# Kernel tuning notes

Measured on AMD Instinct MI355X. Metric: run time of the kernel, lower is better.

## Reference

```python
import jax, jax.numpy as jnp
import numpy as np

B, S, D, H = 4, 2048, 768, 8
HD = D // H
EPS = 1e-5
NEG = -1e9


def setup_inputs() -> dict:
    key = jax.random.key(0)
    ks = jax.random.split(key, 12)
    s = 1.0 / np.sqrt(D)
    inp = {
        "hidden_states": jax.random.normal(ks[0], (B, S, D), dtype=jnp.float32),
        "anchor_mask": jax.random.bernoulli(ks[1], 0.5, (B, S)),
        "ln_g": jnp.ones((D,), jnp.float32),
        "ln_b": jnp.zeros((D,), jnp.float32),
        "Wq": jax.random.uniform(ks[2], (D, D), jnp.float32, -s, s),
        "bq": jax.random.uniform(ks[3], (D,), jnp.float32, -s, s),
        "Wk": jax.random.uniform(ks[4], (D, D), jnp.float32, -s, s),
        "bk": jax.random.uniform(ks[5], (D,), jnp.float32, -s, s),
        "Wv": jax.random.uniform(ks[6], (D, D), jnp.float32, -s, s),
        "bv": jax.random.uniform(ks[7], (D,), jnp.float32, -s, s),
        "Wo": jax.random.uniform(ks[8], (D, D), jnp.float32, -s, s),
        "bo": jax.random.uniform(ks[9], (D,), jnp.float32, -s, s),
    }
    return inp


def reference(hidden_states, anchor_mask, ln_g, ln_b, Wq, bq, Wk, bk, Wv, bv, Wo, bo):
    # LayerNorm (per-token, so applying to all tokens == applying to gathered anchors)
    mu = jnp.mean(hidden_states, axis=-1, keepdims=True)
    var = jnp.mean(jnp.square(hidden_states - mu), axis=-1, keepdims=True)
    x = (hidden_states - mu) * jax.lax.rsqrt(var + EPS) * ln_g + ln_b

    # QKV projections: torch Linear is x @ W.T + b
    q = (jnp.einsum('bsd,ed->bse', x, Wq) + bq).reshape(B, S, H, HD)
    k = (jnp.einsum('bsd,ed->bse', x, Wk) + bk).reshape(B, S, H, HD)
    v = (jnp.einsum('bsd,ed->bse', x, Wv) + bv).reshape(B, S, H, HD)

    scale = 1.0 / np.sqrt(HD)
    scores = jnp.einsum('bqhd,bkhd->bhqk', q, k) * scale
    # keys restricted to anchor positions (equivalent to the gather)
    key_mask = anchor_mask[:, None, None, :]  # (B,1,1,S)
    scores = jnp.where(key_mask, scores, NEG)
    attn = jax.nn.softmax(scores, axis=-1)  # dropout is identity in eval

    out = jnp.einsum('bhqk,bkhd->bqhd', attn, v).reshape(B, S, D)
    out = jnp.einsum('bsd,ed->bse', out, Wo) + bo
    # scatter back: zeros at non-anchor positions
    return out * anchor_mask[:, :, None].astype(out.dtype)
```

## Files before the change

### kernel.cpp

```cpp
#include <hip/hip_runtime.h>
#include <math.h>

#define S_LEN 2048
#define D_DIM 768
#define NH 8
#define HD 96
#define NTOK 8192

typedef short bf16x8 __attribute__((ext_vector_type(8)));
typedef float f32x4 __attribute__((ext_vector_type(4)));
typedef float f32x16 __attribute__((ext_vector_type(16)));
typedef unsigned int u32x2 __attribute__((ext_vector_type(2)));
typedef unsigned int u32x4 __attribute__((ext_vector_type(4)));

__device__ __forceinline__ f32x4 mfma16(bf16x8 a, bf16x8 b, f32x4 c) {
    return __builtin_amdgcn_mfma_f32_16x16x32_bf16(a, b, c, 0, 0, 0);
}
__device__ __forceinline__ f32x16 mfma32(bf16x8 a, bf16x8 b, f32x16 c) {
    return __builtin_amdgcn_mfma_f32_32x32x16_bf16(a, b, c, 0, 0, 0);
}

__device__ __forceinline__ unsigned short f2bf(float f) {
    unsigned int u = __float_as_uint(f);
    u += 0x7fffu + ((u >> 16) & 1u);
    return (unsigned short)(u >> 16);
}

__device__ __forceinline__ unsigned int cvtpk(float lo, float hi) {
    unsigned int r;
    asm("v_cvt_pk_bf16_f32 %0, %1, %2" : "=v"(r) : "v"(lo), "v"(hi));
    return r;
}

__device__ __forceinline__ void gl_lds16(const unsigned short* g, unsigned short* l) {
    __builtin_amdgcn_global_load_lds(
        (const __attribute__((address_space(1))) unsigned int*)g,
        (__attribute__((address_space(3))) unsigned int*)l, 16, 0, 0);
}

#define TILE_SHORTS 6144
#define BH_SHORTS   196608

__global__ __launch_bounds__(256) void prep_kernel(
    const unsigned char* __restrict__ mb, int* __restrict__ idx, int* __restrict__ cnt,
    const float* __restrict__ Wq, const float* __restrict__ Wk,
    const float* __restrict__ Wv, const float* __restrict__ Wo,
    unsigned short* __restrict__ W4b, float* __restrict__ out)
{
    const int bi = blockIdx.x;
    const int t  = threadIdx.x;

    if (bi < 4) {
        __shared__ int red[4];
        __shared__ int warp_tot[4];
        const int b = bi;
        int s = 0;
        for (int i = t; i < NTOK; i += 256) s += (int)mb[i];
        for (int off = 32; off > 0; off >>= 1) s += __shfl_down(s, off, 64);
        if ((t & 63) == 0) red[t >> 6] = s;
        __syncthreads();
        const int total = red[0] + red[1] + red[2] + red[3];
        const int mode = (total > 20000) ? 2 : ((total > 2500) ? 1 : 0);
        const int*   mi = (const int*)mb;
        const float* mf = (const float*)mb;
        const int p0 = t * 8;
        int av = 0, c = 0;
        #pragma unroll
        for (int j = 0; j < 8; ++j) {
            const int g = b * S_LEN + p0 + j;
            bool a;
            if (mode == 2)      a = (mf[g] != 0.0f);
            else if (mode == 1) a = (mb[g] != 0);
            else                a = (mi[g] != 0);
            if (a) { av |= (1 << j); ++c; }
        }
        const int lane = t & 63, w = t >> 6;
        int v = c;
        #pragma unroll
        for (int off = 1; off < 64; off <<= 1) {
            const int u = __shfl_up(v, off, 64);
            if (lane >= off) v += u;
        }
        if (lane == 63) warp_tot[w] = v;
        __syncthreads();
        int wbase = 0;
        for (int i = 0; i < w; ++i) wbase += warp_tot[i];
        int o = wbase + v - c;
        #pragma unroll
        for (int j = 0; j < 8; ++j)
            if (av & (1 << j)) idx[b * S_LEN + (o++)] = p0 + j;
        if (t == 255) cnt[b] = wbase + v;
    } else {
        const int i = bi - 4;
        const int w = i / 288, blk = i % 288;
        const float* src = (w == 0) ? Wq : (w == 1) ? Wk : (w == 2) ? Wv : Wo;
        const int base = (blk * 256 + t) * 8;
        const float4 a = *(const float4*)&src[base];
        const float4 c = *(const float4*)&src[base + 4];
        uint4 u;
        u.x = (unsigned int)f2bf(a.x) | ((unsigned int)f2bf(a.y) << 16);
        u.y = (unsigned int)f2bf(a.z) | ((unsigned int)f2bf(a.w) << 16);
        u.z = (unsigned int)f2bf(c.x) | ((unsigned int)f2bf(c.y) << 16);
        u.w = (unsigned int)f2bf(c.z) | ((unsigned int)f2bf(c.w) << 16);
        *(uint4*)&W4b[(size_t)w * 589824 + base] = u;
    }
}

__global__ __launch_bounds__(256) void ln_gather_kernel(
    const float* __restrict__ H, const float* __restrict__ g,
    const float* __restrict__ bta, const int* __restrict__ idx,
    const int* __restrict__ cnt, unsigned short* __restrict__ X)
{
    const int b = blockIdx.y;
    const int w = threadIdx.x >> 6, lane = threadIdx.x & 63;
    const int r = blockIdx.x * 4 + w;
    if (r >= cnt[b]) return;
    const int slot = b * S_LEN + r;
    const int p = idx[slot];
    const float* hr = H + (size_t)(b * S_LEN + p) * D_DIM;
    unsigned short* xr = X + (size_t)slot * D_DIM;

    float4 v[3];
    #pragma unroll
    for (int q = 0; q < 3; ++q)
        v[q] = *(const float4*)&hr[lane * 4 + q * 256];

    float s = 0.0f, ss = 0.0f;
    #pragma unroll
    for (int q = 0; q < 3; ++q) {
        s  += v[q].x + v[q].y + v[q].z + v[q].w;
        ss += v[q].x * v[q].x + v[q].y * v[q].y
            + v[q].z * v[q].z + v[q].w * v[q].w;
    }
    #pragma unroll
    for (int off = 32; off > 0; off >>= 1) {
        s  += __shfl_xor(s,  off, 64);
        ss += __shfl_xor(ss, off, 64);
    }
    const float mu   = s * (1.0f / D_DIM);
    const float var  = ss * (1.0f / D_DIM) - mu * mu;
    const float rstd = rsqrtf(var + 1e-5f);

    #pragma unroll
    for (int q = 0; q < 3; ++q) {
        const int d0 = lane * 4 + q * 256;
        const float4 gv = *(const float4*)&g[d0];
        const float4 bv = *(const float4*)&bta[d0];
        uint2 u;
        u.x = (unsigned int)f2bf((v[q].x - mu) * rstd * gv.x + bv.x)
            | ((unsigned int)f2bf((v[q].y - mu) * rstd * gv.y + bv.y) << 16);
        u.y = (unsigned int)f2bf((v[q].z - mu) * rstd * gv.z + bv.z)
            | ((unsigned int)f2bf((v[q].w - mu) * rstd * gv.w + bv.w) << 16);
        *(uint2*)&xr[d0] = u;
    }
}

__global__ __launch_bounds__(256) void gemm_bf16(
    const unsigned short* __restrict__ A,
    const unsigned short* __restrict__ W4,
    const float* __restrict__ b0, const float* __restrict__ b1,
    const float* __restrict__ b2,
    const int* __restrict__ cnt, const int* __restrict__ idx,
    unsigned short* __restrict__ Qo, unsigned short* __restrict__ Kp,
    unsigned short* __restrict__ Vp, float* __restrict__ Fo,
    int oproj)
{
    const int bx = blockIdx.x;
    const int z  = oproj ? 0 : (bx % 3);
    const int nx = oproj ? bx : (bx / 3);
    const int m0 = blockIdx.y * 64;
    const int b  = m0 >> 11;
    const int rbase = m0 & (S_LEN - 1);
    const int nc = cnt[b];
    if (rbase >= nc) return;
    const int n0 = nx * 128;
    const unsigned short* W = W4 + (size_t)z * 589824;
    const float* bias = (z == 0) ? b0 : (z == 1 ? b1 : b2);

    __shared__ unsigned short Al[2][64 * 32];
    __shared__ unsigned short Bl[2][128 * 32];

    const int t = threadIdx.x;
    const int srow = t >> 2, sg = t & 3;
    const int ra0 = b * S_LEN + min(rbase + srow, nc - 1);
    const unsigned short* gA0 = A + (size_t)ra0 * 768 + sg * 8;
    const unsigned short* gB0 = W + (size_t)(n0 + srow)      * 768 + sg * 8;
    const unsigned short* gB1 = W + (size_t)(n0 + srow + 64) * 768 + sg * 8;
    const int t8 = t * 8;

    const int w = t >> 6, lane = t & 63;
    const int l15 = lane & 15, quad = lane >> 4;
    const int mh = (w & 1) * 32, nh2 = (w >> 1) * 64;

    f32x4 acc[2][4] = {};

    int aoff[2], boff[4];
    #pragma unroll
    for (int i = 0; i < 2; ++i) aoff[i] = (mh  + i * 16 + l15) * 32 + quad * 8;
    #pragma unroll
    for (int i = 0; i < 4; ++i) boff[i] = (nh2 + i * 16 + l15) * 32 + quad * 8;

    gl_lds16(gA0, &Al[0][t8]);
    gl_lds16(gB0, &Bl[0][t8]);
    gl_lds16(gB1, &Bl[0][2048 + t8]);
    asm volatile("s_waitcnt vmcnt(0)" ::: "memory");
    __builtin_amdgcn_s_barrier();
    __builtin_amdgcn_sched_barrier(0);

    for (int it = 0; it < 24; ++it) {
        const int cur = it & 1;
        if (it + 1 < 24) {
            const int k1 = (it + 1) * 32;
            gl_lds16(gA0 + k1, &Al[cur ^ 1][t8]);
            gl_lds16(gB0 + k1, &Bl[cur ^ 1][t8]);
            gl_lds16(gB1 + k1, &Bl[cur ^ 1][2048 + t8]);
            asm volatile("s_waitcnt vmcnt(3)" ::: "memory");
        } else {
            asm volatile("s_waitcnt vmcnt(0)" ::: "memory");
        }
        __builtin_amdgcn_s_barrier();
        __builtin_amdgcn_sched_barrier(0);

        bf16x8 af[2], bfr[4];
        #pragma unroll
        for (int i = 0; i < 2; ++i) af[i]  = *(const bf16x8*)(&Al[cur][aoff[i]]);
        #pragma unroll
        for (int i = 0; i < 4; ++i) bfr[i] = *(const bf16x8*)(&Bl[cur][boff[i]]);
        #pragma unroll
        for (int ms = 0; ms < 2; ++ms)
            #pragma unroll
            for (int ns = 0; ns < 4; ++ns)
                acc[ms][ns] = mfma16(af[ms], bfr[ns], acc[ms][ns]);

        __builtin_amdgcn_sched_barrier(0);
        __builtin_amdgcn_s_barrier();
    }

    if (!oproj) {
        if (z == 0) {
            #pragma unroll
            for (int ns = 0; ns < 4; ++ns) {
                const int n = n0 + nh2 + ns * 16 + l15;
                const float bv = bias[n];
                #pragma unroll
                for (int ms = 0; ms < 2; ++ms) {
                    const int ml = mh + ms * 16 + quad * 4;
                    #pragma unroll
                    for (int r = 0; r < 4; ++r) {
                        const int slot = b * S_LEN + rbase + ml + r;
                        Qo[(size_t)slot * 768 + n] = f2bf(acc[ms][ns][r] + bv);
                    }
                }
            }
        } else if (z == 1) {
            #pragma unroll
            for (int ns = 0; ns < 4; ++ns) {
                const int n = n0 + nh2 + ns * 16 + l15;
                const int h = n / 96, d = n - h * 96;
                const float bv = bias[n];
                unsigned short* base = Kp + (size_t)(b * 8 + h) * BH_SHORTS;
                const int dseg = d >> 3, dlo = d & 7;
                #pragma unroll
                for (int ms = 0; ms < 2; ++ms) {
                    const int ml = mh + ms * 16 + quad * 4;
                    #pragma unroll
                    for (int r = 0; r < 4; ++r) {
                        const int tok = rbase + ml + r;
                        const int kt = tok >> 6, tk = tok & 63;
                        const int g16 = tk >> 4, lr = tk & 15;
                        base[(size_t)kt * TILE_SHORTS +
                             (g16 * 192 + dseg * 16 + lr) * 8 + dlo] =
                            (tok < nc) ? f2bf(acc[ms][ns][r] + bv)
                                       : (unsigned short)0;
                    }
                }
            }
        } else {
            #pragma unroll
            for (int ns = 0; ns < 4; ++ns) {
                const int n = n0 + nh2 + ns * 16 + l15;
                const int h = n / 96, d = n - h * 96;
                const float bv = bias[n];
                unsigned short* base = Vp + (size_t)(b * 8 + h) * BH_SHORTS;
                const int dg = d >> 4, l16 = d & 15;
                #pragma unroll
                for (int ms = 0; ms < 2; ++ms) {
                    const int ml = mh + ms * 16 + quad * 4;
                    const int k = rbase + ml;
                    const int kt = k >> 6, tk = k & 63;
                    const int kseg = tk >> 3, klo = tk & 7;
                    const unsigned short h0 =
                        (k + 0 < nc) ? f2bf(acc[ms][ns][0] + bv) : (unsigned short)0;
                    const unsigned short h1 =
                        (k + 1 < nc) ? f2bf(acc[ms][ns][1] + bv) : (unsigned short)0;
                    const unsigned short h2 =
                        (k + 2 < nc) ? f2bf(acc[ms][ns][2] + bv) : (unsigned short)0;
                    const unsigned short h3 =
                        (k + 3 < nc) ? f2bf(acc[ms][ns][3] + bv) : (unsigned short)0;
                    uint2 u;
                    u.x = (unsigned int)h0 | ((unsigned int)h1 << 16);
                    u.y = (unsigned int)h2 | ((unsigned int)h3 << 16);
                    *(uint2*)&base[(size_t)kt * TILE_SHORTS +
                                   (dg * 128 + kseg * 16 + l16) * 8 + klo] = u;
                }
            }
        }
    } else {
        #pragma unroll
        for (int ns = 0; ns < 4; ++ns) {
            const int n = n0 + nh2 + ns * 16 + l15;
            const float bv = bias[n];
            #pragma unroll
            for (int ms = 0; ms < 2; ++ms) {
                const int ml = mh + ms * 16 + quad * 4;
                #pragma unroll
                for (int r = 0; r < 4; ++r) {
                    const int rloc = rbase + ml + r;
                    if (rloc < nc) {
                        const int orow = b * S_LEN + idx[b * S_LEN + rloc];
                        Fo[(size_t)orow * 768 + n] = acc[ms][ns][r] + bv;
                    }
                }
            }
        }
    }
}

__global__ __launch_bounds__(256) void attn_mfma(
    const unsigned short* __restrict__ Q,
    const unsigned short* __restrict__ Kp,
    const unsigned short* __restrict__ Vp,
    const int* __restrict__ cnt,
    unsigned short* __restrict__ O)
{
    const int bh = blockIdx.x & 31;
    const int b  = bh >> 3, h = bh & 7;
    const int q0 = (blockIdx.x >> 5) * 32;
    const int nk = cnt[b];
    if (q0 >= nk) return;

    __shared__ f32x4 CMB4[2][64][13];

    const int t = threadIdx.x, w = t >> 6, lane = t & 63;
    const int l15 = lane & 15;
    const int gh  = (lane >> 4) & 1;
    const int hi  = lane >> 5;
    const int q32 = lane & 31;
    const int bS  = b * S_LEN;
    const float CE = 0.14724459f;

    const unsigned short* Kg = Kp + (size_t)(b * 8 + h) * BH_SHORTS;
    const unsigned short* Vg = Vp + (size_t)(b * 8 + h) * BH_SHORTS;

    const unsigned short* qrow = Q + (size_t)(bS + q0 + q32) * 768 + h * 96 + hi * 8;
    bf16x8 qf[6];
    #pragma unroll
    for (int ks = 0; ks < 6; ++ks) qf[ks] = *(const bf16x8*)(qrow + ks * 16);

    const int kb0 = (gh * 192 + hi * 16 + l15) * 8;
    const int vb0 = (gh * 128 + hi * 16 + l15) * 8;

    float ls0 = 0.0f, ls1 = 0.0f;
    f32x16 oacc[3] = {};

    const int kts = (nk + 63) >> 6;

    for (int kt = w; kt < kts; kt += 4) {
        const unsigned short* Kt = Kg + (size_t)kt * TILE_SHORTS + kb0;
        const unsigned short* Vt = Vg + (size_t)kt * TILE_SHORTS + vb0;

        #pragma unroll
        for (int s = 0; s < 2; ++s) {
            bf16x8 kf[6];
            #pragma unroll
            for (int ks = 0; ks < 6; ++ks)
                kf[ks] = *(const bf16x8*)(Kt + (s * 384 + ks * 32) * 8);
            f32x16 sa = {};
            __builtin_amdgcn_s_setprio(1);
            #pragma unroll
            for (int ks = 0; ks < 6; ++ks) sa = mfma32(kf[ks], qf[ks], sa);
            __builtin_amdgcn_s_setprio(0);

            unsigned int wv[8];
            #pragma unroll
            for (int j = 0; j < 8; ++j) {
                const float e0 = exp2f(sa[2 * j]     * CE);
                const float e1 = exp2f(sa[2 * j + 1] * CE);
                if (j & 1) ls1 += e0 + e1; else ls0 += e0 + e1;
                wv[j] = cvtpk(e0, e1);
            }
            const u32x2 r02 = __builtin_amdgcn_permlane32_swap(wv[0], wv[2], false, false);
            const u32x2 r13 = __builtin_amdgcn_permlane32_swap(wv[1], wv[3], false, false);
            const u32x2 r46 = __builtin_amdgcn_permlane32_swap(wv[4], wv[6], false, false);
            const u32x2 r57 = __builtin_amdgcn_permlane32_swap(wv[5], wv[7], false, false);
            const u32x4 pw0 = { r02.x, r13.x, r02.y, r13.y };
            const u32x4 pw1 = { r46.x, r57.x, r46.y, r57.y };
            const bf16x8 pb0 = __builtin_bit_cast(bf16x8, pw0);
            const bf16x8 pb1 = __builtin_bit_cast(bf16x8, pw1);

            const int kkb = s * 2;
            __builtin_amdgcn_s_setprio(1);
            #pragma unroll
            for (int dg = 0; dg < 3; ++dg) {
                const bf16x8 v0 = *(const bf16x8*)(Vt + (dg * 256 + kkb * 32) * 8);
                const bf16x8 v1 = *(const bf16x8*)(Vt + (dg * 256 + (kkb + 1) * 32) * 8);
                oacc[dg] = mfma32(v0, pb0, oacc[dg]);
                oacc[dg] = mfma32(v1, pb1, oacc[dg]);
            }
            __builtin_amdgcn_s_setprio(0);
        }
    }

    float lsum = ls0 + ls1;
    lsum += __shfl_xor(lsum, 32);

    if (w >= 2) {
        f32x4* dst = CMB4[w - 2][lane];
        #pragma unroll
        for (int dg = 0; dg < 3; ++dg)
            #pragma unroll
            for (int m = 0; m < 4; ++m) {
                const f32x4 p = { oacc[dg][4 * m],     oacc[dg][4 * m + 1],
                                  oacc[dg][4 * m + 2], oacc[dg][4 * m + 3] };
                dst[dg * 4 + m] = p;
            }
        const f32x4 tl = { lsum, 0.0f, 0.0f, 0.0f };
        dst[12] = tl;
    }
    __syncthreads();
    if (w < 2) {
        const f32x4* src = CMB4[w][lane];
        #pragma unroll
        for (int dg = 0; dg < 3; ++dg)
            #pragma unroll
            for (int m = 0; m < 4; ++m) {
                const f32x4 p = src[dg * 4 + m];
                #pragma unroll
                for (int j = 0; j < 4; ++j) oacc[dg][4 * m + j] += p[j];
            }
        lsum += src[12][0];
    }
    __syncthreads();
    if (w == 1) {
        f32x4* dst = CMB4[0][lane];
        #pragma unroll
        for (int dg = 0; dg < 3; ++dg)
            #pragma unroll
            for (int m = 0; m < 4; ++m) {
                const f32x4 p = { oacc[dg][4 * m],     oacc[dg][4 * m + 1],
                                  oacc[dg][4 * m + 2], oacc[dg][4 * m + 3] };
                dst[dg * 4 + m] = p;
            }
        const f32x4 tl = { lsum, 0.0f, 0.0f, 0.0f };
        dst[12] = tl;
    }
    __syncthreads();
    if (w > 0) return;

    {
        const f32x4* src = CMB4[0][lane];
        #pragma unroll
        for (int dg = 0; dg < 3; ++dg)
            #pragma unroll
            for (int m = 0; m < 4; ++m) {
                const f32x4 p = src[dg * 4 + m];
                #pragma unroll
                for (int j = 0; j < 4; ++j) oacc[dg][4 * m + j] += p[j];
            }
        lsum += src[12][0];
    }
    lsum -= (float)((kts << 6) - nk);

    const int qi = q0 + q32;
    if (qi < nk) {
        const float rl = 1.0f / lsum;
        unsigned short* og = O + (size_t)(bS + qi) * 768 + h * 96;
        #pragma unroll
        for (int dg = 0; dg < 3; ++dg) {
            #pragma unroll
            for (int m = 0; m < 4; ++m) {
                uint2 u;
                u.x = cvtpk(oacc[dg][4 * m]     * rl, oacc[dg][4 * m + 1] * rl);
                u.y = cvtpk(oacc[dg][4 * m + 2] * rl, oacc[dg][4 * m + 3] * rl);
                *(uint2*)&og[dg * 32 + m * 8 + hi * 4] = u;
            }
        }
    }
}

extern "C" void kernel_launch(void* const* d_in, const int* in_sizes, int n_in,
                              void* d_out, int out_size, void* d_ws, size_t ws_size,
                              hipStream_t stream)
{
    const float* hs  = (const float*)d_in[0];
    const unsigned char* am = (const unsigned char*)d_in[1];
    const float* lng = (const float*)d_in[2];
    const float* lnb = (const float*)d_in[3];
    const float* Wq  = (const float*)d_in[4];
    const float* bq  = (const float*)d_in[5];
    const float* Wk  = (const float*)d_in[6];
    const float* bk  = (const float*)d_in[7];
    const float* Wv  = (const float*)d_in[8];
    const float* bv  = (const float*)d_in[9];
    const float* Wo  = (const float*)d_in[10];
    const float* bo  = (const float*)d_in[11];

    char* ws = (char*)d_ws;
    const size_t BUF = (size_t)NTOK * 768 * 2;
    int* idx = (int*)ws;
    int* cnt = (int*)(ws + 32768);
    unsigned short* xb  = (unsigned short*)(ws + 65536);
    unsigned short* Qb  = (unsigned short*)(ws + 65536 + BUF);
    unsigned short* Kpb = (unsigned short*)(ws + 65536 + 2 * BUF);
    unsigned short* Vpb = (unsigned short*)(ws + 65536 + 3 * BUF);
    unsigned short* W4b = (unsigned short*)(ws + 65536 + 4 * BUF);
    unsigned short* Ob  = xb;
    float* out = (float*)d_out;

    prep_kernel<<<dim3(1156), dim3(256), 0, stream>>>(
        am, idx, cnt, Wq, Wk, Wv, Wo, W4b, out);

    ln_gather_kernel<<<dim3(512, 4), dim3(256), 0, stream>>>(hs, lng, lnb, idx, cnt, xb);

    gemm_bf16<<<dim3(18, 128, 1), dim3(256), 0, stream>>>(
        xb, W4b, bq, bk, bv, cnt, idx, Qb, Kpb, Vpb, nullptr, 0);

    attn_mfma<<<dim3(2048), dim3(256), 0, stream>>>(Qb, Kpb, Vpb, cnt, Ob);

    gemm_bf16<<<dim3(6, 128, 1), dim3(256), 0, stream>>>(
        Ob, W4b + (size_t)3 * 589824, bo, bo, bo, cnt, idx,
        nullptr, nullptr, nullptr, out, 1);
}
```

Measured before the change: 191.2 us.

## Process two 32-query tiles per attention block to reuse K/V fragments

Each attention block now handles 64 query rows, as two 32-row sub-tiles, instead of 32. Every K and V fragment loaded from global memory feeds MFMAs for both sub-tiles, which halves K/V traffic per query. The grid is halved to match. The cost is doubled accumulator and score registers, which may lower occupancy, fewer blocks to balance across CUs, and a larger shared-memory reduction buffer.

```diff
diff --git a/kernel.cpp b/kernel.cpp
--- a/kernel.cpp
+++ b/kernel.cpp
@@ -335,11 +335,11 @@
 {
     const int bh = blockIdx.x & 31;
     const int b  = bh >> 3, h = bh & 7;
-    const int q0 = (blockIdx.x >> 5) * 32;
+    const int q0 = (blockIdx.x >> 5) * 64;
     const int nk = cnt[b];
     if (q0 >= nk) return;
 
-    __shared__ f32x4 CMB4[2][64][13];
+    __shared__ f32x4 CMB4[2][2][64][13];
 
     const int t = threadIdx.x, w = t >> 6, lane = t & 63;
     const int l15 = lane & 15;
@@ -352,16 +352,20 @@
     const unsigned short* Kg = Kp + (size_t)(b * 8 + h) * BH_SHORTS;
     const unsigned short* Vg = Vp + (size_t)(b * 8 + h) * BH_SHORTS;
 
-    const unsigned short* qrow = Q + (size_t)(bS + q0 + q32) * 768 + h * 96 + hi * 8;
-    bf16x8 qf[6];
-    #pragma unroll
-    for (int ks = 0; ks < 6; ++ks) qf[ks] = *(const bf16x8*)(qrow + ks * 16);
+    bf16x8 qf[2][6];
+    #pragma unroll
+    for (int qs = 0; qs < 2; ++qs) {
+        const unsigned short* qrow =
+            Q + (size_t)(bS + q0 + qs * 32 + q32) * 768 + h * 96 + hi * 8;
+        #pragma unroll
+        for (int ks = 0; ks < 6; ++ks) qf[qs][ks] = *(const bf16x8*)(qrow + ks * 16);
+    }
 
     const int kb0 = (gh * 192 + hi * 16 + l15) * 8;
     const int vb0 = (gh * 128 + hi * 16 + l15) * 8;
 
-    float ls0 = 0.0f, ls1 = 0.0f;
-    f32x16 oacc[3] = {};
+    float ls[2][2] = {};
+    f32x16 oacc0[3] = {}, oacc1[3] = {};
 
     const int kts = (nk + 63) >> 6;
 
@@ -375,28 +379,36 @@
             #pragma unroll
             for (int ks = 0; ks < 6; ++ks)
                 kf[ks] = *(const bf16x8*)(Kt + (s * 384 + ks * 32) * 8);
-            f32x16 sa = {};
+            f32x16 sa0 = {}, sa1 = {};
             __builtin_amdgcn_s_setprio(1);
             #pragma unroll
-            for (int ks = 0; ks < 6; ++ks) sa = mfma32(kf[ks], qf[ks], sa);
+            for (int ks = 0; ks < 6; ++ks) {
+                sa0 = mfma32(kf[ks], qf[0][ks], sa0);
+                sa1 = mfma32(kf[ks], qf[1][ks], sa1);
+            }
             __builtin_amdgcn_s_setprio(0);
 
-            unsigned int wv[8];
-            #pragma unroll
-            for (int j = 0; j < 8; ++j) {
-                const float e0 = exp2f(sa[2 * j]     * CE);
-                const float e1 = exp2f(sa[2 * j + 1] * CE);
-                if (j & 1) ls1 += e0 + e1; else ls0 += e0 + e1;
-                wv[j] = cvtpk(e0, e1);
-            }
-            const u32x2 r02 = __builtin_amdgcn_permlane32_swap(wv[0], wv[2], false, false);
-            const u32x2 r13 = __builtin_amdgcn_permlane32_swap(wv[1], wv[3], false, false);
-            const u32x2 r46 = __builtin_amdgcn_permlane32_swap(wv[4], wv[6], false, false);
-            const u32x2 r57 = __builtin_amdgcn_permlane32_swap(wv[5], wv[7], false, false);
-            const u32x4 pw0 = { r02.x, r13.x, r02.y, r13.y };
-            const u32x4 pw1 = { r46.x, r57.x, r46.y, r57.y };
-            const bf16x8 pb0 = __builtin_bit_cast(bf16x8, pw0);
-            const bf16x8 pb1 = __builtin_bit_cast(bf16x8, pw1);
+            bf16x8 pb[2][2];
+            #pragma unroll
+            for (int qs = 0; qs < 2; ++qs) {
+                const f32x16 sa = qs ? sa1 : sa0;
+                unsigned int wv[8];
+                #pragma unroll
+                for (int j = 0; j < 8; ++j) {
+                    const float e0 = exp2f(sa[2 * j]     * CE);
+                    const float e1 = exp2f(sa[2 * j + 1] * CE);
+                    ls[qs][j & 1] += e0 + e1;
+                    wv[j] = cvtpk(e0, e1);
+                }
+                const u32x2 r02 = __builtin_amdgcn_permlane32_swap(wv[0], wv[2], false, false);
+                const u32x2 r13 = __builtin_amdgcn_permlane32_swap(wv[1], wv[3], false, false);
+                const u32x2 r46 = __builtin_amdgcn_permlane32_swap(wv[4], wv[6], false, false);
+                const u32x2 r57 = __builtin_amdgcn_permlane32_swap(wv[5], wv[7], false, false);
+                const u32x4 pw0 = { r02.x, r13.x, r02.y, r13.y };
+                const u32x4 pw1 = { r46.x, r57.x, r46.y, r57.y };
+                pb[qs][0] = __builtin_bit_cast(bf16x8, pw0);
+                pb[qs][1] = __builtin_bit_cast(bf16x8, pw1);
+            }
 
             const int kkb = s * 2;
             __builtin_amdgcn_s_setprio(1);
@@ -404,85 +416,105 @@
             for (int dg = 0; dg < 3; ++dg) {
                 const bf16x8 v0 = *(const bf16x8*)(Vt + (dg * 256 + kkb * 32) * 8);
                 const bf16x8 v1 = *(const bf16x8*)(Vt + (dg * 256 + (kkb + 1) * 32) * 8);
-                oacc[dg] = mfma32(v0, pb0, oacc[dg]);
-                oacc[dg] = mfma32(v1, pb1, oacc[dg]);
+                oacc0[dg] = mfma32(v0, pb[0][0], oacc0[dg]);
+                oacc0[dg] = mfma32(v1, pb[0][1], oacc0[dg]);
+                oacc1[dg] = mfma32(v0, pb[1][0], oacc1[dg]);
+                oacc1[dg] = mfma32(v1, pb[1][1], oacc1[dg]);
             }
             __builtin_amdgcn_s_setprio(0);
         }
     }
 
-    float lsum = ls0 + ls1;
-    lsum += __shfl_xor(lsum, 32);
+    float lsum[2];
+    #pragma unroll
+    for (int qs = 0; qs < 2; ++qs) {
+        lsum[qs] = ls[qs][0] + ls[qs][1];
+        lsum[qs] += __shfl_xor(lsum[qs], 32);
+    }
 
     if (w >= 2) {
-        f32x4* dst = CMB4[w - 2][lane];
-        #pragma unroll
-        for (int dg = 0; dg < 3; ++dg)
-            #pragma unroll
-            for (int m = 0; m < 4; ++m) {
-                const f32x4 p = { oacc[dg][4 * m],     oacc[dg][4 * m + 1],
-                                  oacc[dg][4 * m + 2], oacc[dg][4 * m + 3] };
-                dst[dg * 4 + m] = p;
-            }
-        const f32x4 tl = { lsum, 0.0f, 0.0f, 0.0f };
-        dst[12] = tl;
+        #pragma unroll
+        for (int qs = 0; qs < 2; ++qs) {
+            f32x4* dst = CMB4[qs][w - 2][lane];
+            const f32x16* oa = qs ? oacc1 : oacc0;
+            #pragma unroll
+            for (int dg = 0; dg < 3; ++dg)
+                #pragma unroll
+                for (int m = 0; m < 4; ++m) {
+                    const f32x4 p = { oa[dg][4 * m],     oa[dg][4 * m + 1],
+                                      oa[dg][4 * m + 2], oa[dg][4 * m + 3] };
+                    dst[dg * 4 + m] = p;
+                }
+            const f32x4 tl = { lsum[qs], 0.0f, 0.0f, 0.0f };
+            dst[12] = tl;
+        }
     }
     __syncthreads();
     if (w < 2) {
-        const f32x4* src = CMB4[w][lane];
+        #pragma unroll
+        for (int qs = 0; qs < 2; ++qs) {
+            const f32x4* src = CMB4[qs][w][lane];
+            f32x16* oa = qs ? oacc1 : oacc0;
+            #pragma unroll
+            for (int dg = 0; dg < 3; ++dg)
+                #pragma unroll
+                for (int m = 0; m < 4; ++m) {
+                    const f32x4 p = src[dg * 4 + m];
+                    #pragma unroll
+                    for (int j = 0; j < 4; ++j) oa[dg][4 * m + j] += p[j];
+                }
+            lsum[qs] += src[12][0];
+        }
+    }
+    __syncthreads();
+    if (w == 1) {
+        #pragma unroll
+        for (int qs = 0; qs < 2; ++qs) {
+            f32x4* dst = CMB4[qs][0][lane];
+            const f32x16* oa = qs ? oacc1 : oacc0;
+            #pragma unroll
+            for (int dg = 0; dg < 3; ++dg)
+                #pragma unroll
+                for (int m = 0; m < 4; ++m) {
+                    const f32x4 p = { oa[dg][4 * m],     oa[dg][4 * m + 1],
+                                      oa[dg][4 * m + 2], oa[dg][4 * m + 3] };
+                    dst[dg * 4 + m] = p;
+                }
+            const f32x4 tl = { lsum[qs], 0.0f, 0.0f, 0.0f };
+            dst[12] = tl;
+        }
+    }
+    __syncthreads();
+    if (w > 0) return;
+
+    const float pad = (float)((kts << 6) - nk);
+    #pragma unroll
+    for (int qs = 0; qs < 2; ++qs) {
+        f32x16* oa = qs ? oacc1 : oacc0;
+        const f32x4* src = CMB4[qs][0][lane];
         #pragma unroll
         for (int dg = 0; dg < 3; ++dg)
             #pragma unroll
             for (int m = 0; m < 4; ++m) {
                 const f32x4 p = src[dg * 4 + m];
                 #pragma unroll
-                for (int j = 0; j < 4; ++j) oacc[dg][4 * m + j] += p[j];
-            }
-        lsum += src[12][0];
-    }
-    __syncthreads();
-    if (w == 1) {
-        f32x4* dst = CMB4[0][lane];
-        #pragma unroll
-        for (int dg = 0; dg < 3; ++dg)
-            #pragma unroll
-            for (int m = 0; m < 4; ++m) {
-                const f32x4 p = { oacc[dg][4 * m],     oacc[dg][4 * m + 1],
-                                  oacc[dg][4 * m + 2], oacc[dg][4 * m + 3] };
-                dst[dg * 4 + m] = p;
-            }
-        const f32x4 tl = { lsum, 0.0f, 0.0f, 0.0f };
-        dst[12] = tl;
-    }
-    __syncthreads();
-    if (w > 0) return;
-
-    {
-        const f32x4* src = CMB4[0][lane];
-        #pragma unroll
-        for (int dg = 0; dg < 3; ++dg)
-            #pragma unroll
-            for (int m = 0; m < 4; ++m) {
-                const f32x4 p = src[dg * 4 + m];
-                #pragma unroll
-                for (int j = 0; j < 4; ++j) oacc[dg][4 * m + j] += p[j];
-            }
-        lsum += src[12][0];
-    }
-    lsum -= (float)((kts << 6) - nk);
-
-    const int qi = q0 + q32;
-    if (qi < nk) {
-        const float rl = 1.0f / lsum;
-        unsigned short* og = O + (size_t)(bS + qi) * 768 + h * 96;
-        #pragma unroll
-        for (int dg = 0; dg < 3; ++dg) {
-            #pragma unroll
-            for (int m = 0; m < 4; ++m) {
-                uint2 u;
-                u.x = cvtpk(oacc[dg][4 * m]     * rl, oacc[dg][4 * m + 1] * rl);
-                u.y = cvtpk(oacc[dg][4 * m + 2] * rl, oacc[dg][4 * m + 3] * rl);
-                *(uint2*)&og[dg * 32 + m * 8 + hi * 4] = u;
+                for (int j = 0; j < 4; ++j) oa[dg][4 * m + j] += p[j];
+            }
+        const float lf = lsum[qs] + src[12][0] - pad;
+
+        const int qi = q0 + qs * 32 + q32;
+        if (qi < nk) {
+            const float rl = 1.0f / lf;
+            unsigned short* og = O + (size_t)(bS + qi) * 768 + h * 96;
+            #pragma unroll
+            for (int dg = 0; dg < 3; ++dg) {
+                #pragma unroll
+                for (int m = 0; m < 4; ++m) {
+                    uint2 u;
+                    u.x = cvtpk(oa[dg][4 * m]     * rl, oa[dg][4 * m + 1] * rl);
+                    u.y = cvtpk(oa[dg][4 * m + 2] * rl, oa[dg][4 * m + 3] * rl);
+                    *(uint2*)&og[dg * 32 + m * 8 + hi * 4] = u;
+                }
             }
         }
     }
@@ -525,7 +557,7 @@
     gemm_bf16<<<dim3(18, 128, 1), dim3(256), 0, stream>>>(
         xb, W4b, bq, bk, bv, cnt, idx, Qb, Kpb, Vpb, nullptr, 0);
 
-    attn_mfma<<<dim3(2048), dim3(256), 0, stream>>>(Qb, Kpb, Vpb, cnt, Ob);
+    attn_mfma<<<dim3(1024), dim3(256), 0, stream>>>(Qb, Kpb, Vpb, cnt, Ob);
 
     gemm_bf16<<<dim3(6, 128, 1), dim3(256), 0, stream>>>(
         Ob, W4b + (size_t)3 * 589824, bo, bo, bo, cnt, idx,
```

Result: slower. 218.6 us (+14.3%).
